# Performance work log

Hardware: AMD Instinct MI355X
Metric: run time of the kernel (lower is better)

The kernel has to match this reference:

```python
import jax, jax.numpy as jnp
import numpy as np

S, B, D = 4096, 4, 512  # seq_len, batch, d_model (num_heads = 1, per module's reshape constraint)
THRESH = 0.95           # hard-coded in pasha_max
W_SCALE = 0.05          # keep raw QK^T scores in a range where the threshold mask is non-trivial


def setup_inputs() -> dict:
    key = jax.random.key(0)
    ks = jax.random.split(key, 9)
    return {
        "x":     jax.random.normal(ks[0], (S, B, D), dtype=jnp.float32),
        "q_w":   jax.random.normal(ks[1], (D, D), dtype=jnp.float32) * W_SCALE,
        "q_b":   jax.random.normal(ks[2], (D,),  dtype=jnp.float32) * W_SCALE,
        "k_w":   jax.random.normal(ks[3], (D, D), dtype=jnp.float32) * W_SCALE,
        "k_b":   jax.random.normal(ks[4], (D,),  dtype=jnp.float32) * W_SCALE,
        "v_w":   jax.random.normal(ks[5], (D, D), dtype=jnp.float32) * W_SCALE,
        "v_b":   jax.random.normal(ks[6], (D,),  dtype=jnp.float32) * W_SCALE,
        "out_w": jax.random.normal(ks[7], (D, D), dtype=jnp.float32) * W_SCALE,
        "out_b": jax.random.normal(ks[8], (D,),  dtype=jnp.float32) * W_SCALE,
    }


def reference(x, q_w, q_b, k_w, k_b, v_w, v_b, out_w, out_b):
    # x: [S, B, D] (seq-first, torch MultiheadAttention convention), num_heads = 1
    q = x @ q_w.T + q_b            # [S, B, D]  (NO 1/sqrt(d) scaling: use_pasha_max branch)
    k = x @ k_w.T + k_b
    v = x @ v_w.T + v_b
    qb = q.transpose(1, 0, 2)      # [B, S, D]
    kb = k.transpose(1, 0, 2)
    vb = v.transpose(1, 0, 2)

    scores = jnp.einsum('bsd,btd->bst', qb, kb)  # [B, S_tgt, S_src]

    # pasha_max: one-hot at (first-occurrence) argmax if max >= threshold, else all-zero row.
    max_v = scores.max(axis=-1)                  # [B, S]
    idx = scores.argmax(axis=-1)                 # [B, S] int
    sel_mask = max_v >= THRESH                   # [B, S] bool

    # one_hot @ v is exactly a masked gather of one V row per query -- honor the sparsity.
    gathered = jnp.take_along_axis(vb, idx[..., None], axis=1)   # [B, S, D]
    attn = jnp.where(sel_mask[..., None], gathered, jnp.zeros((), dtype=vb.dtype))

    attn = attn.transpose(1, 0, 2)               # [S, B, D]
    return attn @ out_w.T + out_b
```

## Files before the change

### kernel.cpp

```cpp
#include <hip/hip_runtime.h>
#include <cstdint>
#include <cstddef>

#define S_LEN 4096
#define BATCH 4
#define DMODEL 512
#define THRESHV 0.95f
#define NSPLIT 8
#define NCHUNK (S_LEN / NSPLIT)
#define SBLKS (S_LEN / 128)
#define KSTEPS (DMODEL / 32)

typedef __attribute__((ext_vector_type(8))) short bf16x8;
typedef __attribute__((ext_vector_type(4))) float f32x4;

__device__ __forceinline__ size_t tile_base(int b, int sblk, int kstep) {
    return ((((size_t)b * SBLKS + sblk) * KSTEPS) + kstep) << 12;
}

__device__ __forceinline__ int swz(int row, int slot) {
    return (slot ^ ((row >> 1) & 3)) * 8;
}

__device__ __forceinline__ void gl_lds16(const unsigned short* g, unsigned short* l) {
    __builtin_amdgcn_global_load_lds(
        (const __attribute__((address_space(1))) unsigned int*)g,
        (__attribute__((address_space(3))) unsigned int*)l,
        16, 0, 0);
}

__device__ __forceinline__ void split8_store(const float* __restrict__ g,
                                             unsigned short* __restrict__ ph,
                                             unsigned short* __restrict__ pm,
                                             unsigned short* __restrict__ pl)
{
    const float4 f0 = *(const float4*)g;
    const float4 f1 = *(const float4*)(g + 4);
    const float f[8] = {f0.x, f0.y, f0.z, f0.w, f1.x, f1.y, f1.z, f1.w};
    unsigned int uh[8], um[8], ul[8];
    #pragma unroll
    for (int i = 0; i < 8; ++i) {
        const unsigned int u  = __float_as_uint(f[i]);
        const float e1 = f[i] - __uint_as_float(u & 0xFFFF0000u);
        const unsigned int u1 = __float_as_uint(e1);
        const float e2 = e1 - __uint_as_float(u1 & 0xFFFF0000u);
        uh[i] = u; um[i] = u1; ul[i] = __float_as_uint(e2);
    }
    uint4 wh, wm, wl;
    wh.x = (uh[0] >> 16) | (uh[1] & 0xFFFF0000u);
    wh.y = (uh[2] >> 16) | (uh[3] & 0xFFFF0000u);
    wh.z = (uh[4] >> 16) | (uh[5] & 0xFFFF0000u);
    wh.w = (uh[6] >> 16) | (uh[7] & 0xFFFF0000u);
    wm.x = (um[0] >> 16) | (um[1] & 0xFFFF0000u);
    wm.y = (um[2] >> 16) | (um[3] & 0xFFFF0000u);
    wm.z = (um[4] >> 16) | (um[5] & 0xFFFF0000u);
    wm.w = (um[6] >> 16) | (um[7] & 0xFFFF0000u);
    wl.x = (ul[0] >> 16) | (ul[1] & 0xFFFF0000u);
    wl.y = (ul[2] >> 16) | (ul[3] & 0xFFFF0000u);
    wl.z = (ul[4] >> 16) | (ul[5] & 0xFFFF0000u);
    wl.w = (ul[6] >> 16) | (ul[7] & 0xFFFF0000u);
    *(uint4*)ph = wh; *(uint4*)pm = wm; *(uint4*)pl = wl;
}

__global__ __launch_bounds__(256, 2)
void qkv_mfma_kernel(const float* __restrict__ x,
                     const float* __restrict__ qw, const float* __restrict__ qbias,
                     const float* __restrict__ kw, const float* __restrict__ kbias,
                     const float* __restrict__ vw, const float* __restrict__ vbias,
                     unsigned short* __restrict__ qh_t, unsigned short* __restrict__ qm_t,
                     unsigned short* __restrict__ ql_t, unsigned short* __restrict__ kh_t,
                     unsigned short* __restrict__ km_t, unsigned short* __restrict__ kl_t,
                     unsigned short* __restrict__ vb16)
{
    __shared__ unsigned short Xh[128][32], Xm[128][32], Xl[128][32];
    __shared__ unsigned short Wh[128][32], Wm[128][32], Wl[128][32];

    const int z = blockIdx.z;
    const float* w; const float* bias;
    if (z == 0)      { w = qw; bias = qbias; }
    else if (z == 1) { w = kw; bias = kbias; }
    else             { w = vw; bias = vbias; }
    const bool full6 = (z < 2);

    const int tid = threadIdx.x, lane = tid & 63, wv = tid >> 6;
    const int wrow = (wv >> 1) * 64, wcol = (wv & 1) * 64;
    const int fr = lane & 15, fs = lane >> 4;
    const int m0 = blockIdx.x * 128, n0 = blockIdx.y * 128;

    const int r0s = tid >> 2,         sl0 = tid & 3;
    const int r1s = (tid + 256) >> 2, sl1 = (tid + 256) & 3;

    f32x4 acc[4][4] = {};

    for (int k0 = 0; k0 < DMODEL; k0 += 32) {
        __syncthreads();
        split8_store(x + (size_t)(m0 + r0s) * DMODEL + k0 + sl0 * 8,
                     &Xh[r0s][swz(r0s, sl0)], &Xm[r0s][swz(r0s, sl0)], &Xl[r0s][swz(r0s, sl0)]);
        split8_store(x + (size_t)(m0 + r1s) * DMODEL + k0 + sl1 * 8,
                     &Xh[r1s][swz(r1s, sl1)], &Xm[r1s][swz(r1s, sl1)], &Xl[r1s][swz(r1s, sl1)]);
        split8_store(w + (size_t)(n0 + r0s) * DMODEL + k0 + sl0 * 8,
                     &Wh[r0s][swz(r0s, sl0)], &Wm[r0s][swz(r0s, sl0)], &Wl[r0s][swz(r0s, sl0)]);
        split8_store(w + (size_t)(n0 + r1s) * DMODEL + k0 + sl1 * 8,
                     &Wh[r1s][swz(r1s, sl1)], &Wm[r1s][swz(r1s, sl1)], &Wl[r1s][swz(r1s, sl1)]);
        __syncthreads();

        bf16x8 aH[4], aM[4], aL[4];
        #pragma unroll
        for (int rt = 0; rt < 4; ++rt) {
            const int r = wrow + rt * 16 + fr;
            const int o = swz(r, fs);
            aH[rt] = *(const bf16x8*)&Xh[r][o];
            aM[rt] = *(const bf16x8*)&Xm[r][o];
            if (full6) aL[rt] = *(const bf16x8*)&Xl[r][o];
        }
        #pragma unroll
        for (int ct = 0; ct < 4; ++ct) {
            const int c = wcol + ct * 16 + fr;
            const int o = swz(c, fs);
            const bf16x8 bH = *(const bf16x8*)&Wh[c][o];
            const bf16x8 bM = *(const bf16x8*)&Wm[c][o];
            bf16x8 bL;
            if (full6) bL = *(const bf16x8*)&Wl[c][o];
            #pragma unroll
            for (int rt = 0; rt < 4; ++rt) {
                f32x4 a = acc[rt][ct];
                a = __builtin_amdgcn_mfma_f32_16x16x32_bf16(aH[rt], bH, a, 0, 0, 0);
                a = __builtin_amdgcn_mfma_f32_16x16x32_bf16(aH[rt], bM, a, 0, 0, 0);
                a = __builtin_amdgcn_mfma_f32_16x16x32_bf16(aM[rt], bH, a, 0, 0, 0);
                if (full6) {
                    a = __builtin_amdgcn_mfma_f32_16x16x32_bf16(aM[rt], bM, a, 0, 0, 0);
                    a = __builtin_amdgcn_mfma_f32_16x16x32_bf16(aH[rt], bL, a, 0, 0, 0);
                    a = __builtin_amdgcn_mfma_f32_16x16x32_bf16(aL[rt], bH, a, 0, 0, 0);
                }
                acc[rt][ct] = a;
            }
        }
    }

    if (z < 2) {
        unsigned short* ph = (z == 0) ? qh_t : kh_t;
        unsigned short* pm = (z == 0) ? qm_t : km_t;
        unsigned short* pl = (z == 0) ? ql_t : kl_t;
        #pragma unroll
        for (int ct = 0; ct < 4; ++ct) {
            const int n = n0 + wcol + ct * 16 + fr;
            const float bn = bias[n];
            const int kstep = n >> 5, slot = (n >> 3) & 3, e = n & 7;
            #pragma unroll
            for (int rt = 0; rt < 4; ++rt)
                #pragma unroll
                for (int r = 0; r < 4; ++r) {
                    const int m = m0 + wrow + rt * 16 + fs * 4 + r;
                    const int s = m >> 2, bb = m & 3;
                    const float val = acc[rt][ct][r] + bn;
                    const unsigned int u = __float_as_uint(val);
                    const float e1 = val - __uint_as_float(u & 0xFFFF0000u);
                    const unsigned int u1 = __float_as_uint(e1);
                    const float e2 = e1 - __uint_as_float(u1 & 0xFFFF0000u);
                    const unsigned int u2 = __float_as_uint(e2);
                    const size_t off = tile_base(bb, s >> 7, kstep)
                                     + (size_t)((s & 127) << 5)
                                     + ((slot ^ ((s >> 1) & 3)) << 3) + e;
                    ph[off] = (unsigned short)(u >> 16);
                    pm[off] = (unsigned short)(u1 >> 16);
                    pl[off] = (unsigned short)(u2 >> 16);
                }
        }
    } else {
        #pragma unroll
        for (int ct = 0; ct < 4; ++ct) {
            const int n = n0 + wcol + ct * 16 + fr;
            const float bn = bias[n];
            #pragma unroll
            for (int rt = 0; rt < 4; ++rt)
                #pragma unroll
                for (int r = 0; r < 4; ++r) {
                    const int m = m0 + wrow + rt * 16 + fs * 4 + r;
                    const int s = m >> 2, bb = m & 3;
                    const float val = acc[rt][ct][r] + bn;
                    const unsigned int u = __float_as_uint(val);
                    vb16[((size_t)bb * S_LEN + s) * DMODEL + n] =
                        (unsigned short)((u + 0x7FFFu + ((u >> 16) & 1u)) >> 16);
                }
        }
    }
}

__global__ __launch_bounds__(256, 3)
void score_argmax_kernel(const unsigned short* __restrict__ qh, const unsigned short* __restrict__ qm,
                         const unsigned short* __restrict__ ql, const unsigned short* __restrict__ kh,
                         const unsigned short* __restrict__ km, const unsigned short* __restrict__ kl,
                         float* __restrict__ pmax, int* __restrict__ pidx)
{
    __shared__ unsigned short Qh[4096], Qm[4096], Ql[4096];
    __shared__ unsigned short Kh[4096], Km[4096], Kl[4096];
    __shared__ float redM[4][64];
    __shared__ int   redI[4][64];

    const int tid = threadIdx.x, lane = tid & 63, wv = tid >> 6;
    const int wrow = (wv >> 1) * 64, wcol = (wv & 1) * 64;
    const int fr = lane & 15, fs = lane >> 4;

    const int b = blockIdx.y, sblk = blockIdx.x, s0 = sblk * 128;
    const int to = tid << 3;

    float rmax[16]; int ridx[16];
    #pragma unroll
    for (int s = 0; s < 16; ++s) { rmax[s] = -3.0e38f; ridx[s] = 0; }

    for (int nt = 0; nt < NCHUNK / 128; ++nt) {
        const int tblk = blockIdx.z * (NCHUNK / 128) + nt;
        const int trow0 = tblk * 128;
        f32x4 acc[4][4] = {};

        for (int kstep = 0; kstep < KSTEPS; ++kstep) {
            __syncthreads();
            const size_t qb = tile_base(b, sblk, kstep) + to;
            const size_t kb = tile_base(b, tblk, kstep) + to;
            gl_lds16(qh + qb,        &Qh[to]);
            gl_lds16(qm + qb,        &Qm[to]);
            gl_lds16(ql + qb,        &Ql[to]);
            gl_lds16(kh + kb,        &Kh[to]);
            gl_lds16(km + kb,        &Km[to]);
            gl_lds16(kl + kb,        &Kl[to]);
            gl_lds16(qh + qb + 2048, &Qh[to + 2048]);
            gl_lds16(qm + qb + 2048, &Qm[to + 2048]);
            gl_lds16(ql + qb + 2048, &Ql[to + 2048]);
            gl_lds16(kh + kb + 2048, &Kh[to + 2048]);
            gl_lds16(km + kb + 2048, &Km[to + 2048]);
            gl_lds16(kl + kb + 2048, &Kl[to + 2048]);
            __syncthreads();

            bf16x8 aH[4], aM[4], aL[4];
            #pragma unroll
            for (int rt = 0; rt < 4; ++rt) {
                const int r = wrow + rt * 16 + fr;
                const int o = r * 32 + swz(r, fs);
                aH[rt] = *(const bf16x8*)&Qh[o];
                aM[rt] = *(const bf16x8*)&Qm[o];
                aL[rt] = *(const bf16x8*)&Ql[o];
            }
            #pragma unroll
            for (int ct = 0; ct < 4; ++ct) {
                const int c = wcol + ct * 16 + fr;
                const int o = c * 32 + swz(c, fs);
                const bf16x8 bH = *(const bf16x8*)&Kh[o];
                const bf16x8 bM = *(const bf16x8*)&Km[o];
                const bf16x8 bL = *(const bf16x8*)&Kl[o];
                #pragma unroll
                for (int rt = 0; rt < 4; ++rt) {
                    f32x4 a = acc[rt][ct];
                    a = __builtin_amdgcn_mfma_f32_16x16x32_bf16(aH[rt], bH, a, 0, 0, 0);
                    a = __builtin_amdgcn_mfma_f32_16x16x32_bf16(aH[rt], bM, a, 0, 0, 0);
                    a = __builtin_amdgcn_mfma_f32_16x16x32_bf16(aM[rt], bH, a, 0, 0, 0);
                    a = __builtin_amdgcn_mfma_f32_16x16x32_bf16(aM[rt], bM, a, 0, 0, 0);
                    a = __builtin_amdgcn_mfma_f32_16x16x32_bf16(aH[rt], bL, a, 0, 0, 0);
                    a = __builtin_amdgcn_mfma_f32_16x16x32_bf16(aL[rt], bH, a, 0, 0, 0);
                    acc[rt][ct] = a;
                }
            }
        }

        #pragma unroll
        for (int rt = 0; rt < 4; ++rt)
            #pragma unroll
            for (int ct = 0; ct < 4; ++ct) {
                const int t = trow0 + wcol + ct * 16 + fr;
                #pragma unroll
                for (int r = 0; r < 4; ++r) {
                    const float sc = acc[rt][ct][r];
                    if (sc > rmax[rt * 4 + r]) { rmax[rt * 4 + r] = sc; ridx[rt * 4 + r] = t; }
                }
            }
    }

    #pragma unroll
    for (int s = 0; s < 16; ++s) {
        float mv = rmax[s]; int ii = ridx[s];
        #pragma unroll
        for (int off = 1; off < 16; off <<= 1) {
            const float om = __shfl_xor(mv, off, 64);
            const int   oi = __shfl_xor(ii, off, 64);
            if (om > mv || (om == mv && oi < ii)) { mv = om; ii = oi; }
        }
        if (fr == 0) {
            const int row_local = (s >> 2) * 16 + fs * 4 + (s & 3);
            redM[wv][row_local] = mv;
            redI[wv][row_local] = ii;
        }
    }
    __syncthreads();

    if ((wv & 1) == 0) {
        const float m0v = redM[wv][lane];
        const float m1v = redM[wv + 1][lane];
        const int   i0v = redI[wv][lane];
        const int   i1v = redI[wv + 1][lane];
        float mv = m0v; int ii = i0v;
        if (m1v > mv || (m1v == mv && i1v < ii)) { mv = m1v; ii = i1v; }
        const int row = s0 + wrow + lane;
        const size_t o = ((size_t)b * S_LEN + row) * NSPLIT + blockIdx.z;
        pmax[o] = mv; pidx[o] = ii;
    }
}

__global__ __launch_bounds__(256)
void gather_proj_kernel(const unsigned short* __restrict__ v,
                        const float* __restrict__ ow, const float* __restrict__ obias,
                        const float* __restrict__ pmax, const int* __restrict__ pidx,
                        float* __restrict__ out)
{
    constexpr int BM = 64, BN = 64, BK = 32;
    __shared__ float As[BK][BM + 4];
    __shared__ float Bs[BK][BN + 4];
    __shared__ int sidx[BM];

    const int tid = threadIdx.x;
    const int tx = tid & 15, ty = tid >> 4;
    const int m0 = blockIdx.x * BM;
    const int n0 = blockIdx.y * BN;
    const int lr = tid >> 3;
    const int lc = (tid & 7) << 2;

    if (tid < BM) {
        const int m = m0 + tid;
        const int s = m >> 2, b = m & 3;
        const float* pm = pmax + ((size_t)b * S_LEN + s) * NSPLIT;
        const int*   pi = pidx + ((size_t)b * S_LEN + s) * NSPLIT;
        float best = pm[0]; int bi = pi[0];
        #pragma unroll
        for (int c = 1; c < NSPLIT; ++c)
            if (pm[c] > best) { best = pm[c]; bi = pi[c]; }
        sidx[tid] = (best >= THRESHV) ? bi : -1;
    }
    __syncthreads();

    float acc[4][4] = {};

    for (int k0 = 0; k0 < DMODEL; k0 += BK) {
        const int i0 = sidx[lr];
        const int i1 = sidx[lr + 32];
        const int b0r = (m0 + lr) & 3;
        const int b1r = (m0 + lr + 32) & 3;
        float4 a0 = make_float4(0.f, 0.f, 0.f, 0.f);
        float4 a1 = make_float4(0.f, 0.f, 0.f, 0.f);
        if (i0 >= 0) {
            const uint2 rw = *(const uint2*)(v + ((size_t)b0r * S_LEN + i0) * DMODEL + k0 + lc);
            a0.x = __uint_as_float(rw.x << 16); a0.y = __uint_as_float(rw.x & 0xFFFF0000u);
            a0.z = __uint_as_float(rw.y << 16); a0.w = __uint_as_float(rw.y & 0xFFFF0000u);
        }
        if (i1 >= 0) {
            const uint2 rw = *(const uint2*)(v + ((size_t)b1r * S_LEN + i1) * DMODEL + k0 + lc);
            a1.x = __uint_as_float(rw.x << 16); a1.y = __uint_as_float(rw.x & 0xFFFF0000u);
            a1.z = __uint_as_float(rw.y << 16); a1.w = __uint_as_float(rw.y & 0xFFFF0000u);
        }
        const float4 w0 = *(const float4*)(ow + (size_t)(n0 + lr)      * DMODEL + k0 + lc);
        const float4 w1 = *(const float4*)(ow + (size_t)(n0 + lr + 32) * DMODEL + k0 + lc);
        As[lc+0][lr]    = a0.x; As[lc+1][lr]    = a0.y; As[lc+2][lr]    = a0.z; As[lc+3][lr]    = a0.w;
        As[lc+0][lr+32] = a1.x; As[lc+1][lr+32] = a1.y; As[lc+2][lr+32] = a1.z; As[lc+3][lr+32] = a1.w;
        Bs[lc+0][lr]    = w0.x; Bs[lc+1][lr]    = w0.y; Bs[lc+2][lr]    = w0.z; Bs[lc+3][lr]    = w0.w;
        Bs[lc+0][lr+32] = w1.x; Bs[lc+1][lr+32] = w1.y; Bs[lc+2][lr+32] = w1.z; Bs[lc+3][lr+32] = w1.w;
        __syncthreads();
        #pragma unroll
        for (int kk = 0; kk < BK; ++kk) {
            const float4 av = *(const float4*)&As[kk][ty << 2];
            const float4 bv = *(const float4*)&Bs[kk][tx << 2];
            const float a[4] = {av.x, av.y, av.z, av.w};
            const float bb[4] = {bv.x, bv.y, bv.z, bv.w};
            #pragma unroll
            for (int i = 0; i < 4; ++i)
                #pragma unroll
                for (int j = 0; j < 4; ++j)
                    acc[i][j] = fmaf(a[i], bb[j], acc[i][j]);
        }
        __syncthreads();
    }

    const float4 biasv = *(const float4*)(obias + n0 + (tx << 2));
    #pragma unroll
    for (int i = 0; i < 4; ++i) {
        const int m = m0 + (ty << 2) + i;
        float4 r;
        r.x = acc[i][0] + biasv.x;
        r.y = acc[i][1] + biasv.y;
        r.z = acc[i][2] + biasv.z;
        r.w = acc[i][3] + biasv.w;
        *(float4*)(out + (size_t)m * DMODEL + n0 + (tx << 2)) = r;
    }
}

extern "C" void kernel_launch(void* const* d_in, const int* in_sizes, int n_in,
                              void* d_out, int out_size, void* d_ws, size_t ws_size,
                              hipStream_t stream)
{
    const float* x  = (const float*)d_in[0];
    const float* qw = (const float*)d_in[1];
    const float* qbias = (const float*)d_in[2];
    const float* kw = (const float*)d_in[3];
    const float* kbias = (const float*)d_in[4];
    const float* vw = (const float*)d_in[5];
    const float* vbias = (const float*)d_in[6];
    const float* ow = (const float*)d_in[7];
    const float* obias = (const float*)d_in[8];
    float* out = (float*)d_out;

    const size_t SBD = (size_t)S_LEN * BATCH * DMODEL;
    unsigned short* qh_t = (unsigned short*)d_ws;
    unsigned short* qm_t = qh_t + SBD;
    unsigned short* ql_t = qm_t + SBD;
    unsigned short* kh_t = ql_t + SBD;
    unsigned short* km_t = kh_t + SBD;
    unsigned short* kl_t = km_t + SBD;
    unsigned short* vb16 = kl_t + SBD;
    float* pmax = (float*)(vb16 + SBD);
    int*   pidx = (int*)(pmax + (size_t)BATCH * S_LEN * NSPLIT);

    dim3 g1(128, 4, 3);
    qkv_mfma_kernel<<<g1, 256, 0, stream>>>(x, qw, qbias, kw, kbias, vw, vbias,
                                            qh_t, qm_t, ql_t, kh_t, km_t, kl_t, vb16);

    dim3 g2(S_LEN / 128, BATCH, NSPLIT);
    score_argmax_kernel<<<g2, 256, 0, stream>>>(qh_t, qm_t, ql_t, kh_t, km_t, kl_t, pmax, pidx);

    dim3 g3((S_LEN * BATCH) / 64, DMODEL / 64);
    gather_proj_kernel<<<g3, 256, 0, stream>>>(vb16, ow, obias, pmax, pidx, out);
}
```

Baseline: 677.1 us.

## Double-buffer Q/K LDS tiles in score-argmax kernel to overlap loads with MFMA

Splits the Q and K shared-memory tiles into two buffers and flattens the tile and k-step loops into one step loop. The next step's tile is prefetched into the other buffer while MFMAs run on the current one, so each step needs one barrier instead of two. This doubles LDS use to about 96KB per block and drops the occupancy hint in launch bounds, which may cut resident blocks per CU.

```diff
diff --git a/kernel.cpp b/kernel.cpp
--- a/kernel.cpp
+++ b/kernel.cpp
@@ -186,14 +186,14 @@
     }
 }
 
-__global__ __launch_bounds__(256, 3)
+__global__ __launch_bounds__(256)
 void score_argmax_kernel(const unsigned short* __restrict__ qh, const unsigned short* __restrict__ qm,
                          const unsigned short* __restrict__ ql, const unsigned short* __restrict__ kh,
                          const unsigned short* __restrict__ km, const unsigned short* __restrict__ kl,
                          float* __restrict__ pmax, int* __restrict__ pidx)
 {
-    __shared__ unsigned short Qh[4096], Qm[4096], Ql[4096];
-    __shared__ unsigned short Kh[4096], Km[4096], Kl[4096];
+    __shared__ unsigned short Qh[2][4096], Qm[2][4096], Ql[2][4096];
+    __shared__ unsigned short Kh[2][4096], Km[2][4096], Kl[2][4096];
     __shared__ float redM[4][64];
     __shared__ int   redI[4][64];
 
@@ -203,75 +203,89 @@
 
     const int b = blockIdx.y, sblk = blockIdx.x, s0 = sblk * 128;
     const int to = tid << 3;
+    const int NT = NCHUNK / 128;
+    const int tblk0 = blockIdx.z * NT;
+
+    auto stage = [&](int step, int bi) {
+        const int nt_ = step >> 4, ks_ = step & 15;
+        const size_t qb = tile_base(b, sblk, ks_) + to;
+        const size_t kb = tile_base(b, tblk0 + nt_, ks_) + to;
+        gl_lds16(qh + qb,        &Qh[bi][to]);
+        gl_lds16(qm + qb,        &Qm[bi][to]);
+        gl_lds16(ql + qb,        &Ql[bi][to]);
+        gl_lds16(kh + kb,        &Kh[bi][to]);
+        gl_lds16(km + kb,        &Km[bi][to]);
+        gl_lds16(kl + kb,        &Kl[bi][to]);
+        gl_lds16(qh + qb + 2048, &Qh[bi][to + 2048]);
+        gl_lds16(qm + qb + 2048, &Qm[bi][to + 2048]);
+        gl_lds16(ql + qb + 2048, &Ql[bi][to + 2048]);
+        gl_lds16(kh + kb + 2048, &Kh[bi][to + 2048]);
+        gl_lds16(km + kb + 2048, &Km[bi][to + 2048]);
+        gl_lds16(kl + kb + 2048, &Kl[bi][to + 2048]);
+    };
 
     float rmax[16]; int ridx[16];
     #pragma unroll
     for (int s = 0; s < 16; ++s) { rmax[s] = -3.0e38f; ridx[s] = 0; }
 
-    for (int nt = 0; nt < NCHUNK / 128; ++nt) {
-        const int tblk = blockIdx.z * (NCHUNK / 128) + nt;
-        const int trow0 = tblk * 128;
-        f32x4 acc[4][4] = {};
-
-        for (int kstep = 0; kstep < KSTEPS; ++kstep) {
-            __syncthreads();
-            const size_t qb = tile_base(b, sblk, kstep) + to;
-            const size_t kb = tile_base(b, tblk, kstep) + to;
-            gl_lds16(qh + qb,        &Qh[to]);
-            gl_lds16(qm + qb,        &Qm[to]);
-            gl_lds16(ql + qb,        &Ql[to]);
-            gl_lds16(kh + kb,        &Kh[to]);
-            gl_lds16(km + kb,        &Km[to]);
-            gl_lds16(kl + kb,        &Kl[to]);
-            gl_lds16(qh + qb + 2048, &Qh[to + 2048]);
-            gl_lds16(qm + qb + 2048, &Qm[to + 2048]);
-            gl_lds16(ql + qb + 2048, &Ql[to + 2048]);
-            gl_lds16(kh + kb + 2048, &Kh[to + 2048]);
-            gl_lds16(km + kb + 2048, &Km[to + 2048]);
-            gl_lds16(kl + kb + 2048, &Kl[to + 2048]);
-            __syncthreads();
-
-            bf16x8 aH[4], aM[4], aL[4];
+    f32x4 acc[4][4] = {};
+    stage(0, 0);
+
+    for (int step = 0; step < NT * KSTEPS; ++step) {
+        const int cur = step & 1;
+        const int ks  = step & 15;
+        const int nt  = step >> 4;
+        __syncthreads();
+        if (step + 1 < NT * KSTEPS) stage(step + 1, cur ^ 1);
+
+        bf16x8 aH[4], aM[4], aL[4];
+        #pragma unroll
+        for (int rt = 0; rt < 4; ++rt) {
+            const int r = wrow + rt * 16 + fr;
+            const int o = r * 32 + swz(r, fs);
+            aH[rt] = *(const bf16x8*)&Qh[cur][o];
+            aM[rt] = *(const bf16x8*)&Qm[cur][o];
+            aL[rt] = *(const bf16x8*)&Ql[cur][o];
+        }
+        #pragma unroll
+        for (int ct = 0; ct < 4; ++ct) {
+            const int c = wcol + ct * 16 + fr;
+            const int o = c * 32 + swz(c, fs);
+            const bf16x8 bH = *(const bf16x8*)&Kh[cur][o];
+            const bf16x8 bM = *(const bf16x8*)&Km[cur][o];
+            const bf16x8 bL = *(const bf16x8*)&Kl[cur][o];
             #pragma unroll
             for (int rt = 0; rt < 4; ++rt) {
-                const int r = wrow + rt * 16 + fr;
-                const int o = r * 32 + swz(r, fs);
-                aH[rt] = *(const bf16x8*)&Qh[o];
-                aM[rt] = *(const bf16x8*)&Qm[o];
-                aL[rt] = *(const bf16x8*)&Ql[o];
+                f32x4 a = acc[rt][ct];
+                a = __builtin_amdgcn_mfma_f32_16x16x32_bf16(aH[rt], bH, a, 0, 0, 0);
+                a = __builtin_amdgcn_mfma_f32_16x16x32_bf16(aH[rt], bM, a, 0, 0, 0);
+                a = __builtin_amdgcn_mfma_f32_16x16x32_bf16(aM[rt], bH, a, 0, 0, 0);
+                a = __builtin_amdgcn_mfma_f32_16x16x32_bf16(aM[rt], bM, a, 0, 0, 0);
+                a = __builtin_amdgcn_mfma_f32_16x16x32_bf16(aH[rt], bL, a, 0, 0, 0);
+                a = __builtin_amdgcn_mfma_f32_16x16x32_bf16(aL[rt], bH, a, 0, 0, 0);
+                acc[rt][ct] = a;
             }
-            #pragma unroll
-            for (int ct = 0; ct < 4; ++ct) {
-                const int c = wcol + ct * 16 + fr;
-                const int o = c * 32 + swz(c, fs);
-                const bf16x8 bH = *(const bf16x8*)&Kh[o];
-                const bf16x8 bM = *(const bf16x8*)&Km[o];
-                const bf16x8 bL = *(const bf16x8*)&Kl[o];
+        }
+
+        if (ks == KSTEPS - 1) {
+            const int trow0 = (tblk0 + nt) * 128;
+            #pragma unroll
+            for (int rt = 0; rt < 4; ++rt)
                 #pragma unroll
-                for (int rt = 0; rt < 4; ++rt) {
-                    f32x4 a = acc[rt][ct];
-                    a = __builtin_amdgcn_mfma_f32_16x16x32_bf16(aH[rt], bH, a, 0, 0, 0);
-                    a = __builtin_amdgcn_mfma_f32_16x16x32_bf16(aH[rt], bM, a, 0, 0, 0);
-                    a = __builtin_amdgcn_mfma_f32_16x16x32_bf16(aM[rt], bH, a, 0, 0, 0);
-                    a = __builtin_amdgcn_mfma_f32_16x16x32_bf16(aM[rt], bM, a, 0, 0, 0);
-                    a = __builtin_amdgcn_mfma_f32_16x16x32_bf16(aH[rt], bL, a, 0, 0, 0);
-                    a = __builtin_amdgcn_mfma_f32_16x16x32_bf16(aL[rt], bH, a, 0, 0, 0);
-                    acc[rt][ct] = a;
+                for (int ct = 0; ct < 4; ++ct) {
+                    const int t = trow0 + wcol + ct * 16 + fr;
+                    #pragma unroll
+                    for (int r = 0; r < 4; ++r) {
+                        const float sc = acc[rt][ct][r];
+                        if (sc > rmax[rt * 4 + r]) { rmax[rt * 4 + r] = sc; ridx[rt * 4 + r] = t; }
+                    }
                 }
-            }
-        }
-
-        #pragma unroll
-        for (int rt = 0; rt < 4; ++rt)
-            #pragma unroll
-            for (int ct = 0; ct < 4; ++ct) {
-                const int t = trow0 + wcol + ct * 16 + fr;
+            #pragma unroll
+            for (int rt = 0; rt < 4; ++rt)
                 #pragma unroll
-                for (int r = 0; r < 4; ++r) {
-                    const float sc = acc[rt][ct][r];
-                    if (sc > rmax[rt * 4 + r]) { rmax[rt * 4 + r] = sc; ridx[rt * 4 + r] = t; }
-                }
-            }
+                for (int ct = 0; ct < 4; ++ct)
+                    acc[rt][ct] = (f32x4){0.f, 0.f, 0.f, 0.f};
+        }
     }
 
     #pragma unroll
```

After: 817.9 us. +20.8%, slower.
